# Kernel optimization log

Hardware: AMD Instinct MI355X
Metric: run time of the kernel (lower is better)

## Reference

```python
import jax, jax.numpy as jnp
import numpy as np

DIM = 512
N = 1024
DIM_HEAD = 64
HEADS = 8
BATCH = 8
SCALE = DIM_HEAD ** -0.5


def setup_inputs() -> dict:
    key = jax.random.key(0)
    ks = jax.random.split(key, 9)
    s = 0.02
    return {
        "x": jax.random.normal(ks[0], (BATCH, N, DIM), dtype=jnp.float32),
        "w_qkv": jax.random.normal(ks[1], (3 * DIM, DIM), dtype=jnp.float32) * s,
        "b_qkv": jax.random.normal(ks[2], (3 * DIM,), dtype=jnp.float32) * s,
        "wq": jax.random.normal(ks[3], (N, DIM_HEAD), dtype=jnp.float32) * s,
        "bq": jax.random.normal(ks[4], (N,), dtype=jnp.float32) * s,
        "wk": jax.random.normal(ks[5], (N, DIM_HEAD), dtype=jnp.float32) * s,
        "bk": jax.random.normal(ks[6], (N,), dtype=jnp.float32) * s,
        "w_out": jax.random.normal(ks[7], (DIM, DIM), dtype=jnp.float32) * s,
        "b_out": jax.random.normal(ks[8], (DIM,), dtype=jnp.float32) * s,
    }


def _split_heads(t):
    # [b, n, h*d] -> [b, h, n, d]
    b, n, _ = t.shape
    return t.reshape(b, n, HEADS, DIM_HEAD).transpose(0, 2, 1, 3)


def reference(x, w_qkv, b_qkv, wq, bq, wk, bk, w_out, b_out):
    # fused QKV projection: [b, n, 3*dim]
    qkv = x @ w_qkv.T + b_qkv
    qo, ko, vo = jnp.split(qkv, 3, axis=-1)
    q, k, v = _split_heads(qo), _split_heads(ko), _split_heads(vo)  # [b,h,n,d]

    # additive-attention stage 1: A = softmax(Wq(q) * scale) over last dim
    A = jax.nn.softmax((jnp.einsum('bhnd,md->bhnm', q, wq) + bq) * SCALE, axis=-1)  # [b,h,n,n]
    q_global = jnp.sum(jnp.einsum('bhnm,bhmd->bhnd', A, q), axis=-1, keepdims=True)  # [b,h,n,1]
    p = q_global * k  # [b,h,n,d]

    # stage 2
    B = jax.nn.softmax((jnp.einsum('bhnd,md->bhnm', p, wk) + bk) * SCALE, axis=-1)  # [b,h,n,n]
    k_global = jnp.sum(jnp.einsum('bhnm,bhmd->bhnd', B, p), axis=-1, keepdims=True)  # [b,h,n,1]

    u = (k_global * v).transpose(0, 2, 1, 3).reshape(x.shape[0], N, DIM)  # [b,n,dim]
    out = u @ w_out.T + b_out + qo
    return out
```

## Files before the change

kernel.cpp:

```cpp
#include <hip/hip_runtime.h>


#define SCL2 0.1803368801f
typedef unsigned short u16;
typedef __attribute__((ext_vector_type(8))) short short8;
typedef __attribute__((ext_vector_type(4))) float f32x4;

#define MFMA16(a, b, c) __builtin_amdgcn_mfma_f32_16x16x32_bf16((a), (b), (c), 0, 0, 0)

__device__ __forceinline__ float bf2f(u16 u) {
    union { unsigned int i; float f; } v; v.i = ((unsigned int)u) << 16; return v.f;
}
__device__ __forceinline__ u16 f2bf(float f) {
    union { float f; unsigned int i; } v; v.f = f;
    unsigned int x = v.i;
    return (u16)((x + 0x7FFFu + ((x >> 16) & 1u)) >> 16);
}

__device__ __forceinline__ void gload16(const u16* g, u16* l) {
    __builtin_amdgcn_global_load_lds(
        (__attribute__((address_space(1))) void*)(void*)g,
        (__attribute__((address_space(3))) void*)l, 16, 0, 0);
}

__global__ __launch_bounds__(256) void conv_kernel(
    const float* __restrict__ w_qkv, const float* __restrict__ w_out,
    const float* __restrict__ wq, const float* __restrict__ wk,
    const float* __restrict__ x, u16* __restrict__ wsb)
{
    const int idx = (blockIdx.x * 256 + threadIdx.x) * 4;
    const float* src; int off;
    if      (idx < 786432)  { src = w_qkv; off = idx; }
    else if (idx < 1048576) { src = w_out; off = idx - 786432; }
    else if (idx < 1114112) { src = wq;    off = idx - 1048576; }
    else if (idx < 1179648) { src = wk;    off = idx - 1114112; }
    else                    { src = x;     off = idx - 1179648; }
    float4 v = *(const float4*)(src + off);
    ushort4 o; o.x = f2bf(v.x); o.y = f2bf(v.y); o.z = f2bf(v.z); o.w = f2bf(v.w);
    *(ushort4*)(wsb + idx) = o;
}

#define MQK 0
#define MVU 1
#define MOUT 2

template <int MODE, int NCT>
__global__ __launch_bounds__(256) void gemm_k(
    const u16* __restrict__ Ab, int lda, int acol,
    const u16* __restrict__ Wb, const float* __restrict__ bias,
    const float* __restrict__ kg, const u16* __restrict__ qkws_ro,
    u16* __restrict__ qkws, float* __restrict__ outp,
    float* __restrict__ qsout, float* __restrict__ ksout)
{
    constexpr int BN = NCT * 16;
    constexpr int CST = BN + 8;
    constexpr int ASZ = 128 * 64;
    constexpr int BSZ = BN * 64;
    constexpr int HALF = ASZ + BSZ;
    constexpr int CELEM = 128 * CST;
    constexpr int SMSZ = (2 * HALF > HALF + CELEM) ? 2 * HALF : HALF + CELEM;
    __shared__ u16 sm[SMSZ];
    u16* const Cb = sm + HALF;

    const int t = threadIdx.x;
    const int w = t >> 6, lane = t & 63, s = lane & 15, quad = lane >> 4;
    const int sx = lane & 7;

    const int nwgy = gridDim.y;
    const int nwg = gridDim.x * nwgy;
    const int flat = blockIdx.y * gridDim.x + blockIdx.x;
    const int swz = (flat & 7) * (nwg >> 3) + (flat >> 3);
    const int by = swz % nwgy, bx = swz / nwgy;
    const int bm = bx * 128, jn0 = by * BN;

    const int r8 = lane >> 3;
    const int c8x = ((lane & 7) ^ r8) << 3;

    f32x4 acc[2][NCT];
#pragma unroll
    for (int i = 0; i < 2; ++i)
#pragma unroll
        for (int j = 0; j < NCT; ++j) acc[i][j] = (f32x4){0.f, 0.f, 0.f, 0.f};

    const u16* ga = Ab + (size_t)(bm + w * 32 + r8) * lda + acol + c8x;
    const u16* gb = Wb + (size_t)(jn0 + w * (NCT * 4) + r8) * 512 + c8x;

    auto stage = [&](int buf, int kt) {
        u16* la = sm + buf * HALF + (w * 32) * 64;
        u16* lb = sm + buf * HALF + ASZ + (w * (NCT * 4)) * 64;
#pragma unroll
        for (int j = 0; j < 4; ++j)
            gload16(ga + (size_t)j * 8 * lda + kt, la + j * 8 * 64);
#pragma unroll
        for (int j = 0; j < NCT / 2; ++j)
            gload16(gb + (size_t)j * 8 * 512 + kt, lb + j * 8 * 64);
    };
    auto compute = [&](int buf) {
        const u16* Ab_ = sm + buf * HALF;
        const u16* Bb_ = Ab_ + ASZ;
#pragma unroll
        for (int kk = 0; kk < 2; ++kk) {
            const int ca = ((kk * 4 + quad) ^ sx) << 3;
            short8 a0 = *(const short8*)&Ab_[(w * 32 + s) * 64 + ca];
            short8 a1 = *(const short8*)&Ab_[(w * 32 + 16 + s) * 64 + ca];
#pragma unroll
            for (int ct = 0; ct < NCT; ++ct) {
                short8 bf = *(const short8*)&Bb_[(ct * 16 + s) * 64 + ca];
                acc[0][ct] = MFMA16(a0, bf, acc[0][ct]);
                acc[1][ct] = MFMA16(a1, bf, acc[1][ct]);
            }
        }
    };

    stage(1, 0);
    __syncthreads();
#pragma unroll
    for (int it = 0; it < 7; ++it) {
        const int cur = 1 - (it & 1);
        stage(1 - cur, 64 * (it + 1));
        __builtin_amdgcn_sched_barrier(0);
        compute(cur);
        __syncthreads();
    }
    compute(0);

    if constexpr (MODE == MOUT) {
#pragma unroll
        for (int mt = 0; mt < 2; ++mt)
#pragma unroll
            for (int ct = 0; ct < NCT; ++ct) {
                const int jn = jn0 + ct * 16 + s;
#pragma unroll
                for (int r = 0; r < 4; ++r) {
                    const int row = bm + w * 32 + mt * 16 + quad * 4 + r;
                    outp[(size_t)row * 512 + jn] =
                        acc[mt][ct][r] + bias[jn] + bf2f(qkws_ro[(size_t)row * 1024 + jn]);
                }
            }
    } else {
        float rsum[2][NCT / 4][4];
        if constexpr (MODE == MQK) {
#pragma unroll
            for (int mt = 0; mt < 2; ++mt)
#pragma unroll
                for (int hg = 0; hg < NCT / 4; ++hg)
#pragma unroll
                    for (int r = 0; r < 4; ++r) rsum[mt][hg][r] = 0.f;
        }
        __syncthreads();
#pragma unroll
        for (int mt = 0; mt < 2; ++mt)
#pragma unroll
            for (int ct = 0; ct < NCT; ++ct) {
                const int jn = jn0 + ct * 16 + s;
                const float bj = bias[jn];
#pragma unroll
                for (int r = 0; r < 4; ++r) {
                    const int rowl = w * 32 + mt * 16 + quad * 4 + r;
                    float v = acc[mt][ct][r] + bj;
                    if constexpr (MODE == MVU) {
                        const int row = bm + rowl;
                        v *= kg[(((row >> 10) * 8 + (jn >> 6)) << 10) | (row & 1023)];
                    }
                    if constexpr (MODE == MQK) rsum[mt][ct >> 2][r] += v;
                    Cb[rowl * CST + ct * 16 + s] = f2bf(v);
                }
            }
        if constexpr (MODE == MQK) {
#pragma unroll
            for (int mt = 0; mt < 2; ++mt)
#pragma unroll
                for (int hg = 0; hg < NCT / 4; ++hg)
#pragma unroll
                    for (int r = 0; r < 4; ++r) {
                        float S = rsum[mt][hg][r];
                        S += __shfl_xor(S, 1);
                        S += __shfl_xor(S, 2);
                        S += __shfl_xor(S, 4);
                        S += __shfl_xor(S, 8);
                        if (s == 0) {
                            const int row = bm + w * 32 + mt * 16 + quad * 4 + r;
                            const int jj = jn0 + hg * 64;
                            float* dst = (jj < 512) ? qsout : ksout;
                            dst[((((row >> 10) << 3) | ((jj >> 6) & 7)) << 10) | (row & 1023)] = S;
                        }
                    }
        }
        __syncthreads();
        const int row = t >> 1, ch = (t & 1) * (NCT * 8);
        u16* dp = qkws + (size_t)(bm + row) * 1024 + (MODE == MVU ? 512 : 0) + jn0 + ch;
#pragma unroll
        for (int i = 0; i < NCT; ++i)
            *(uint4*)(dp + i * 8) = *(const uint4*)&Cb[row * CST + ch + i * 8];
    }
}

template <int STG>
__global__ __launch_bounds__(512) void stage_gemm(
    const u16* __restrict__ qkws, int qcol0,
    const u16* __restrict__ wmb, const float* __restrict__ biasv,
    const float* __restrict__ rowscale,
    const float* __restrict__ wv1, const float* __restrict__ wv2,
    float* __restrict__ outg)
{
    __shared__ u16 sm[24576];
    __shared__ float zp[2][128], wp[2][128];
    u16* const As = sm;

    const int t = threadIdx.x;
    const int w = t >> 6, lane = t & 63, s = lane & 15, quad = lane >> 4;
    const int sx = lane & 7;
    const int r8 = lane >> 3;
    const int c8x = ((lane & 7) ^ r8) << 3;
    const int wr = w & 3;
    const int mg = w >> 2;

    const int flat = blockIdx.y * gridDim.x + blockIdx.x;
    const int swz = (flat & 7) * 64 + (flat >> 3);
    const int h = swz & 7, bx = swz >> 3;
    const int bm = bx * 128;
    const int bh = ((bm >> 10) << 3) + h;
    const int n0 = bm & 1023;

    const u16* gA = qkws + (size_t)(bm + w * 16 + r8) * 1024 + qcol0 + (h << 6) + c8x;
    const u16* gB = wmb + (size_t)(w * 16 + r8) * 64 + c8x;

    auto stageB = [&](int buf, int c) {
        u16* lb = sm + 8192 + buf * 8192 + (w * 16) * 64;
        const u16* g = gB + (size_t)c * 128 * 64;
#pragma unroll
        for (int j = 0; j < 2; ++j)
            gload16(g + (size_t)j * 8 * 64, lb + j * 8 * 64);
    };

#pragma unroll
    for (int j = 0; j < 2; ++j)
        gload16(gA + (size_t)j * 8 * 1024, As + (w * 16 + j * 8) * 64);
    stageB(1, 0);
    __syncthreads();

    short8 a[2][2];
#pragma unroll
    for (int nt = 0; nt < 2; ++nt)
#pragma unroll
        for (int kk = 0; kk < 2; ++kk)
            a[nt][kk] = *(const short8*)&As[(wr * 32 + nt * 16 + s) * 64 + (((kk * 4 + quad) ^ sx) << 3)];

    float rsf[2][4];
#pragma unroll
    for (int nt = 0; nt < 2; ++nt)
#pragma unroll
        for (int r = 0; r < 4; ++r) {
            if constexpr (STG == 2)
                rsf[nt][r] = rowscale[(bh << 10) + n0 + wr * 32 + nt * 16 + quad * 4 + r] * SCL2;
            else
                rsf[nt][r] = SCL2;
        }

    float z[2][4] = {}, wacc[2][4] = {};
    const int ct0 = mg * 4;

#pragma unroll 1
    for (int c = 0; c < 8; ++c) {
        const int cur = 1 - (c & 1);
        if (c < 7) stageB(1 - cur, c + 1);
        __builtin_amdgcn_sched_barrier(0);

        float bmv[4], wvv[4];
#pragma unroll
        for (int i = 0; i < 4; ++i) {
            const int m = c * 128 + (ct0 + i) * 16 + s;
            bmv[i] = biasv[m] * SCL2;
            float wv = wv1[(bh << 10) + m];
            if constexpr (STG == 2) wv *= wv2[(bh << 10) + m];
            wvv[i] = wv;
        }

        const u16* Bb = sm + 8192 + cur * 8192;
#pragma unroll
        for (int i = 0; i < 4; ++i) {
            const int ct = ct0 + i;
            const short8 b0 = *(const short8*)&Bb[(ct * 16 + s) * 64 + ((quad ^ sx) << 3)];
            const short8 b1 = *(const short8*)&Bb[(ct * 16 + s) * 64 + (((4 + quad) ^ sx) << 3)];
#pragma unroll
            for (int nt = 0; nt < 2; ++nt) {
                f32x4 acc = (f32x4){0.f, 0.f, 0.f, 0.f};
                acc = MFMA16(a[nt][0], b0, acc);
                acc = MFMA16(a[nt][1], b1, acc);
#pragma unroll
                for (int r = 0; r < 4; ++r) {
                    const float e = __builtin_amdgcn_exp2f(rsf[nt][r] * acc[r] + bmv[i]);
                    z[nt][r] += e;
                    wacc[nt][r] += e * wvv[i];
                }
            }
        }
        __syncthreads();
    }

#pragma unroll
    for (int nt = 0; nt < 2; ++nt)
#pragma unroll
        for (int r = 0; r < 4; ++r) {
            float Z = z[nt][r], W = wacc[nt][r];
            for (int off = 1; off < 16; off <<= 1) {
                Z += __shfl_xor(Z, off);
                W += __shfl_xor(W, off);
            }
            if (s == 0) {
                const int rowl = wr * 32 + nt * 16 + quad * 4 + r;
                zp[mg][rowl] = Z;
                wp[mg][rowl] = W;
            }
        }
    __syncthreads();
    if (t < 128) {
        const float Z = zp[0][t] + zp[1][t];
        const float W = wp[0][t] + wp[1][t];
        outg[(bh << 10) + n0 + t] = W / Z;
    }
}

extern "C" void kernel_launch(void* const* d_in, const int* in_sizes, int n_in,
                              void* d_out, int out_size, void* d_ws, size_t ws_size,
                              hipStream_t stream)
{
    const float* x     = (const float*)d_in[0];
    const float* w_qkv = (const float*)d_in[1];
    const float* b_qkv = (const float*)d_in[2];
    const float* wq    = (const float*)d_in[3];
    const float* bq    = (const float*)d_in[4];
    const float* wk    = (const float*)d_in[5];
    const float* bk    = (const float*)d_in[6];
    const float* w_out = (const float*)d_in[7];
    const float* b_out = (const float*)d_in[8];
    float* out = (float*)d_out;

    float* qs = (float*)d_ws;
    float* ks = qs + 65536;
    float* qg = ks + 65536;
    float* kg = qg + 65536;
    u16* wsb   = (u16*)(kg + 65536);
    u16* wqkvb = wsb;
    u16* woutb = wqkvb + 786432;
    u16* wqb   = woutb + 262144;
    u16* wkb   = wqb + 65536;
    u16* xb    = wkb + 65536;
    u16* qkws  = xb + 4194304;

    conv_kernel<<<5248, 256, 0, stream>>>(w_qkv, w_out, wq, wk, x, wsb);
    gemm_k<MQK, 8><<<dim3(64, 8), 256, 0, stream>>>(
        xb, 512, 0, wqkvb, b_qkv, nullptr, nullptr, qkws, nullptr, qs, ks);
    stage_gemm<1><<<dim3(64, 8), 512, 0, stream>>>(
        qkws, 0, wqb, bq, nullptr, qs, nullptr, qg);
    stage_gemm<2><<<dim3(64, 8), 512, 0, stream>>>(
        qkws, 512, wkb, bk, qg, qg, ks, kg);
    gemm_k<MVU, 4><<<dim3(64, 8), 256, 0, stream>>>(
        xb, 512, 0, wqkvb + (size_t)1024 * 512, b_qkv + 1024, kg, nullptr, qkws,
        nullptr, nullptr, nullptr);
    gemm_k<MOUT, 4><<<dim3(64, 8), 256, 0, stream>>>(
        qkws, 1024, 512, woutb, b_out, nullptr, qkws, nullptr, out, nullptr, nullptr);
}
```

Measured before the change: 163.2 us.

## Fold k_global scaling into output GEMM and compute V in QKV GEMM

```diff
diff --git a/kernel.cpp b/kernel.cpp
--- a/kernel.cpp
+++ b/kernel.cpp
@@ -41,14 +41,13 @@
 }
 
 #define MQK 0
-#define MVU 1
 #define MOUT 2
 
 template <int MODE, int NCT>
 __global__ __launch_bounds__(256) void gemm_k(
     const u16* __restrict__ Ab, int lda, int acol,
     const u16* __restrict__ Wb, const float* __restrict__ bias,
-    const float* __restrict__ kg, const u16* __restrict__ qkws_ro,
+    const float* __restrict__ kg, const u16* __restrict__ qkws_ro, int ldq,
     u16* __restrict__ qkws, float* __restrict__ outp,
     float* __restrict__ qsout, float* __restrict__ ksout)
 {
@@ -76,12 +75,6 @@
     const int r8 = lane >> 3;
     const int c8x = ((lane & 7) ^ r8) << 3;
 
-    f32x4 acc[2][NCT];
-#pragma unroll
-    for (int i = 0; i < 2; ++i)
-#pragma unroll
-        for (int j = 0; j < NCT; ++j) acc[i][j] = (f32x4){0.f, 0.f, 0.f, 0.f};
-
     const u16* ga = Ab + (size_t)(bm + w * 32 + r8) * lda + acol + c8x;
     const u16* gb = Wb + (size_t)(jn0 + w * (NCT * 4) + r8) * 512 + c8x;
 
@@ -95,7 +88,7 @@
         for (int j = 0; j < NCT / 2; ++j)
             gload16(gb + (size_t)j * 8 * 512 + kt, lb + j * 8 * 64);
     };
-    auto compute = [&](int buf) {
+    auto compute = [&](int buf, f32x4 (&ac)[2][NCT]) {
         const u16* Ab_ = sm + buf * HALF;
         const u16* Bb_ = Ab_ + ASZ;
 #pragma unroll
@@ -106,47 +99,39 @@
 #pragma unroll
             for (int ct = 0; ct < NCT; ++ct) {
                 short8 bf = *(const short8*)&Bb_[(ct * 16 + s) * 64 + ca];
-                acc[0][ct] = MFMA16(a0, bf, acc[0][ct]);
-                acc[1][ct] = MFMA16(a1, bf, acc[1][ct]);
+                ac[0][ct] = MFMA16(a0, bf, ac[0][ct]);
+                ac[1][ct] = MFMA16(a1, bf, ac[1][ct]);
             }
         }
     };
 
-    stage(1, 0);
-    __syncthreads();
-#pragma unroll
-    for (int it = 0; it < 7; ++it) {
-        const int cur = 1 - (it & 1);
-        stage(1 - cur, 64 * (it + 1));
-        __builtin_amdgcn_sched_barrier(0);
-        compute(cur);
-        __syncthreads();
-    }
-    compute(0);
-
-    if constexpr (MODE == MOUT) {
+    if constexpr (MODE == MQK) {
+        f32x4 acc[2][NCT];
+#pragma unroll
+        for (int i = 0; i < 2; ++i)
+#pragma unroll
+            for (int j = 0; j < NCT; ++j) acc[i][j] = (f32x4){0.f, 0.f, 0.f, 0.f};
+
+        stage(1, 0);
+        __syncthreads();
+#pragma unroll
+        for (int it = 0; it < 7; ++it) {
+            const int cur = 1 - (it & 1);
+            stage(1 - cur, 64 * (it + 1));
+            __builtin_amdgcn_sched_barrier(0);
+            compute(cur, acc);
+            __syncthreads();
+        }
+        compute(0, acc);
+
+        float rsum[2][NCT / 4][4];
 #pragma unroll
         for (int mt = 0; mt < 2; ++mt)
 #pragma unroll
-            for (int ct = 0; ct < NCT; ++ct) {
-                const int jn = jn0 + ct * 16 + s;
-#pragma unroll
-                for (int r = 0; r < 4; ++r) {
-                    const int row = bm + w * 32 + mt * 16 + quad * 4 + r;
-                    outp[(size_t)row * 512 + jn] =
-                        acc[mt][ct][r] + bias[jn] + bf2f(qkws_ro[(size_t)row * 1024 + jn]);
-                }
-            }
-    } else {
-        float rsum[2][NCT / 4][4];
-        if constexpr (MODE == MQK) {
-#pragma unroll
-            for (int mt = 0; mt < 2; ++mt)
-#pragma unroll
-                for (int hg = 0; hg < NCT / 4; ++hg)
-#pragma unroll
-                    for (int r = 0; r < 4; ++r) rsum[mt][hg][r] = 0.f;
-        }
+            for (int hg = 0; hg < NCT / 4; ++hg)
+#pragma unroll
+                for (int r = 0; r < 4; ++r) rsum[mt][hg][r] = 0.f;
+
         __syncthreads();
 #pragma unroll
         for (int mt = 0; mt < 2; ++mt)
@@ -158,19 +143,16 @@
                 for (int r = 0; r < 4; ++r) {
                     const int rowl = w * 32 + mt * 16 + quad * 4 + r;
                     float v = acc[mt][ct][r] + bj;
-                    if constexpr (MODE == MVU) {
-                        const int row = bm + rowl;
-                        v *= kg[(((row >> 10) * 8 + (jn >> 6)) << 10) | (row & 1023)];
-                    }
-                    if constexpr (MODE == MQK) rsum[mt][ct >> 2][r] += v;
+                    rsum[mt][ct >> 2][r] += v;
                     Cb[rowl * CST + ct * 16 + s] = f2bf(v);
                 }
             }
-        if constexpr (MODE == MQK) {
-#pragma unroll
-            for (int mt = 0; mt < 2; ++mt)
-#pragma unroll
-                for (int hg = 0; hg < NCT / 4; ++hg)
+#pragma unroll
+        for (int mt = 0; mt < 2; ++mt)
+#pragma unroll
+            for (int hg = 0; hg < NCT / 4; ++hg) {
+                const int jj = jn0 + hg * 64;
+                if (jj < 1024) {
 #pragma unroll
                     for (int r = 0; r < 4; ++r) {
                         float S = rsum[mt][hg][r];
@@ -180,18 +162,69 @@
                         S += __shfl_xor(S, 8);
                         if (s == 0) {
                             const int row = bm + w * 32 + mt * 16 + quad * 4 + r;
-                            const int jj = jn0 + hg * 64;
                             float* dst = (jj < 512) ? qsout : ksout;
                             dst[((((row >> 10) << 3) | ((jj >> 6) & 7)) << 10) | (row & 1023)] = S;
                         }
                     }
-        }
+                }
+            }
         __syncthreads();
         const int row = t >> 1, ch = (t & 1) * (NCT * 8);
-        u16* dp = qkws + (size_t)(bm + row) * 1024 + (MODE == MVU ? 512 : 0) + jn0 + ch;
+        u16* dp = qkws + (size_t)(bm + row) * ldq + jn0 + ch;
 #pragma unroll
         for (int i = 0; i < NCT; ++i)
             *(uint4*)(dp + i * 8) = *(const uint4*)&Cb[row * CST + ch + i * 8];
+    } else {
+        f32x4 tot[2][NCT];
+#pragma unroll
+        for (int i = 0; i < 2; ++i)
+#pragma unroll
+            for (int j = 0; j < NCT; ++j) tot[i][j] = (f32x4){0.f, 0.f, 0.f, 0.f};
+
+        const float* kgb = kg + ((bm >> 10) * 8 << 10) + (bm & 1023)
+                              + w * 32 + quad * 4;
+
+        stage(1, 0);
+        __syncthreads();
+#pragma unroll 1
+        for (int it = 0; it < 8; ++it) {
+            const int cur = 1 - (it & 1);
+            if (it < 7) stage(1 - cur, 64 * (it + 1));
+            float kgr[2][4];
+#pragma unroll
+            for (int mt = 0; mt < 2; ++mt)
+#pragma unroll
+                for (int r = 0; r < 4; ++r)
+                    kgr[mt][r] = kgb[(it << 10) + mt * 16 + r];
+            __builtin_amdgcn_sched_barrier(0);
+            f32x4 acc[2][NCT];
+#pragma unroll
+            for (int i = 0; i < 2; ++i)
+#pragma unroll
+                for (int j = 0; j < NCT; ++j) acc[i][j] = (f32x4){0.f, 0.f, 0.f, 0.f};
+            compute(cur, acc);
+#pragma unroll
+            for (int mt = 0; mt < 2; ++mt)
+#pragma unroll
+                for (int ct = 0; ct < NCT; ++ct)
+#pragma unroll
+                    for (int r = 0; r < 4; ++r)
+                        tot[mt][ct][r] += kgr[mt][r] * acc[mt][ct][r];
+            __syncthreads();
+        }
+
+#pragma unroll
+        for (int mt = 0; mt < 2; ++mt)
+#pragma unroll
+            for (int ct = 0; ct < NCT; ++ct) {
+                const int jn = jn0 + ct * 16 + s;
+#pragma unroll
+                for (int r = 0; r < 4; ++r) {
+                    const int row = bm + w * 32 + mt * 16 + quad * 4 + r;
+                    outp[(size_t)row * 512 + jn] =
+                        tot[mt][ct][r] + bias[jn] + bf2f(qkws_ro[(size_t)row * ldq + jn]);
+                }
+            }
     }
 }
 
@@ -222,7 +255,7 @@
     const int bh = ((bm >> 10) << 3) + h;
     const int n0 = bm & 1023;
 
-    const u16* gA = qkws + (size_t)(bm + w * 16 + r8) * 1024 + qcol0 + (h << 6) + c8x;
+    const u16* gA = qkws + (size_t)(bm + w * 16 + r8) * 1536 + qcol0 + (h << 6) + c8x;
     const u16* gB = wmb + (size_t)(w * 16 + r8) * 64 + c8x;
 
     auto stageB = [&](int buf, int c) {
@@ -235,7 +268,7 @@
 
 #pragma unroll
     for (int j = 0; j < 2; ++j)
-        gload16(gA + (size_t)j * 8 * 1024, As + (w * 16 + j * 8) * 64);
+        gload16(gA + (size_t)j * 8 * 1536, As + (w * 16 + j * 8) * 64);
     stageB(1, 0);
     __syncthreads();
 
@@ -349,15 +382,13 @@
     u16* qkws  = xb + 4194304;
 
     conv_kernel<<<5248, 256, 0, stream>>>(w_qkv, w_out, wq, wk, x, wsb);
-    gemm_k<MQK, 8><<<dim3(64, 8), 256, 0, stream>>>(
-        xb, 512, 0, wqkvb, b_qkv, nullptr, nullptr, qkws, nullptr, qs, ks);
+    gemm_k<MQK, 8><<<dim3(64, 12), 256, 0, stream>>>(
+        xb, 512, 0, wqkvb, b_qkv, nullptr, nullptr, 1536, qkws, nullptr, qs, ks);
     stage_gemm<1><<<dim3(64, 8), 512, 0, stream>>>(
         qkws, 0, wqb, bq, nullptr, qs, nullptr, qg);
     stage_gemm<2><<<dim3(64, 8), 512, 0, stream>>>(
         qkws, 512, wkb, bk, qg, qg, ks, kg);
-    gemm_k<MVU, 4><<<dim3(64, 8), 256, 0, stream>>>(
-        xb, 512, 0, wqkvb + (size_t)1024 * 512, b_qkv + 1024, kg, nullptr, qkws,
-        nullptr, nullptr, nullptr);
     gemm_k<MOUT, 4><<<dim3(64, 8), 256, 0, stream>>>(
-        qkws, 1024, 512, woutb, b_out, nullptr, qkws, nullptr, out, nullptr, nullptr);
-}
+        qkws, 1536, 1024, woutb, b_out, kg, qkws, 1536, nullptr, out,
+        nullptr, nullptr);
+}
```

After: 169.3 us. 1.04x slower.
